# Optimization experiments

Measured on AMD Instinct MI355X. Metric: run time of the kernel, lower is better.

Reference implementation:

```python
import jax, jax.numpy as jnp
import numpy as np

D_MODEL = 512
N_HEADS = 8
HEAD_DIM = D_MODEL // N_HEADS
MAX_LEN = 250  # relative table has 2*MAX_LEN-1 = 499 rows
B, L = 2, 2048


def setup_inputs() -> dict:
    rng = jax.random.key(0)
    ks = jax.random.split(rng, 10)
    w = 1.0 / np.sqrt(D_MODEL)
    return {
        "query": jax.random.normal(ks[0], (B, L, D_MODEL), jnp.float32),
        "key": jax.random.normal(ks[1], (B, L, D_MODEL), jnp.float32),
        "value": jax.random.normal(ks[2], (B, L, D_MODEL), jnp.float32),
        "mask": jax.random.randint(ks[3], (B, L), 0, 2, jnp.int32),
        # weights stored as [in, out]; apply as x @ W + b (equivalent to torch Linear)
        "Wq": jax.random.normal(ks[4], (D_MODEL, D_MODEL), jnp.float32) * w,
        "bq": jnp.zeros((D_MODEL,), jnp.float32),
        "Wk": jax.random.normal(ks[5], (D_MODEL, D_MODEL), jnp.float32) * w,
        "bk": jnp.zeros((D_MODEL,), jnp.float32),
        "Wv": jax.random.normal(ks[6], (D_MODEL, D_MODEL), jnp.float32) * w,
        "bv": jnp.zeros((D_MODEL,), jnp.float32),
        "Wo": jax.random.normal(ks[7], (D_MODEL, D_MODEL), jnp.float32) * w,
        "bo": jnp.zeros((D_MODEL,), jnp.float32),
        "rel_table": jax.random.normal(ks[8], (2 * MAX_LEN - 1, HEAD_DIM), jnp.float32),
    }


def reference(query, key, value, mask, Wq, bq, Wk, bk, Wv, bv, Wo, bo, rel_table):
    b, l, d = query.shape
    hd = d // N_HEADS

    def split_heads(x):  # [b,l,d] -> [b,h,l,hd]
        return x.reshape(b, l, N_HEADS, hd).transpose(0, 2, 1, 3)

    Q = split_heads(query @ Wq + bq)
    K = split_heads(key @ Wk + bk)
    V = split_heads(value @ Wv + bv)

    scores = jnp.einsum('bhid,bhjd->bhij', Q, K) / jnp.sqrt(jnp.float32(hd))

    # relative position indices: idx[i,j] = clamp(j - i + MAX_LEN-1, 0, 2*MAX_LEN-2)
    pos = jnp.arange(l)
    idx = jnp.clip(pos[None, :] - pos[:, None] + MAX_LEN - 1, 0, 2 * MAX_LEN - 2)
    rel = rel_table[idx]  # [l, l, hd] gather
    # Shaw-style additive relative-position bias (per-pair scalar from Q . rel)
    scores = scores + jnp.einsum('bhid,ijd->bhij', Q, rel)

    # key-padding mask: [b,l] -> [b,1,1,l]
    scores = jnp.where(mask[:, None, None, :] == 0, jnp.float32(-1e10), scores)

    weights = jax.nn.softmax(scores, axis=-1)  # [b,h,l,l]
    out = jnp.einsum('bhij,bhjd->bhid', weights, V)
    out = out.transpose(0, 2, 1, 3).reshape(b, l, d)
    return out @ Wo + bo
```

## Files before the change

### kernel.cpp

```cpp
#include <hip/hip_runtime.h>
#include <math.h>

#define NREL 499
#define NREL_PAD 500
#define LDB 72
#define LDT 72

typedef __attribute__((ext_vector_type(8))) short bf16x8;
typedef __attribute__((ext_vector_type(4))) float f32x4;

__device__ __forceinline__ float bf2f(ushort x) {
  union { unsigned u; float f; } v; v.u = ((unsigned)x) << 16; return v.f;
}
__device__ __forceinline__ ushort f2bf(float x) {
  union { float f; unsigned u; } v; v.f = x;
  return (ushort)((v.u + 0x8000u) >> 16);
}
__device__ __forceinline__ bf16x8 pack8(float4 a, float4 b) {
  bf16x8 r;
  r[0] = (short)f2bf(a.x); r[1] = (short)f2bf(a.y);
  r[2] = (short)f2bf(a.z); r[3] = (short)f2bf(a.w);
  r[4] = (short)f2bf(b.x); r[5] = (short)f2bf(b.y);
  r[6] = (short)f2bf(b.z); r[7] = (short)f2bf(b.w);
  return r;
}

__global__ __launch_bounds__(256) void cast_bf16(const float* __restrict__ q,
                                                 const float* __restrict__ k,
                                                 const float* __restrict__ v,
                                                 ushort* __restrict__ dst) {
  const int z = blockIdx.z;
  const float* src = (z == 0) ? q : (z == 1) ? k : v;
  const size_t base = ((size_t)blockIdx.x * 256 + threadIdx.x) * 8;
  float4 a = *(const float4*)(src + base);
  float4 b = *(const float4*)(src + base + 4);
  *(bf16x8*)(dst + (size_t)z * 2097152 + base) = pack8(a, b);
}

__global__ __launch_bounds__(256) void prep_wt(const float* __restrict__ W0,
                                               const float* __restrict__ W1,
                                               const float* __restrict__ W2,
                                               const float* __restrict__ W3,
                                               const int* __restrict__ mask,
                                               ushort* __restrict__ Wt,
                                               ushort* __restrict__ maskbf) {
  __shared__ float T[64][68];
  const int t = threadIdx.x;
  const int k0 = blockIdx.x * 64, n0 = blockIdx.y * 64, z = blockIdx.z;
  const float* W = (z == 0) ? W0 : (z == 1) ? W1 : (z == 2) ? W2 : W3;
#pragma unroll
  for (int s = 0; s < 4; ++s) {
    int idx = t + s * 256;
    int r = idx >> 4, c4 = (idx & 15) << 2;
    *(float4*)&T[r][c4] = *(const float4*)(W + (size_t)(k0 + r) * 512 + n0 + c4);
  }
  if (blockIdx.x == 0 && blockIdx.y == 0) {
    int base = z * 1024 + t * 4;
    int4 mv = *(const int4*)(mask + base);
    ushort4 mo;
    mo.x = mv.x ? 0x3F80 : 0; mo.y = mv.y ? 0x3F80 : 0;
    mo.z = mv.z ? 0x3F80 : 0; mo.w = mv.w ? 0x3F80 : 0;
    *(ushort4*)(maskbf + base) = mo;
  }
  __syncthreads();
#pragma unroll
  for (int s = 0; s < 4; ++s) {
    int idx = t + s * 256;
    int row = idx >> 4, c4 = (idx & 15) << 2;
    ushort4 u = make_ushort4(f2bf(T[c4 + 0][row]), f2bf(T[c4 + 1][row]),
                             f2bf(T[c4 + 2][row]), f2bf(T[c4 + 3][row]));
    *(ushort4*)(Wt + (size_t)z * 262144 + (size_t)(n0 + row) * 512 + k0 + c4) = u;
  }
}

template <int MODE>
__device__ __forceinline__ void gemm_tile_body(const ushort* __restrict__ A,
                                               const ushort* __restrict__ Wt,
                                               const float* __restrict__ bias,
                                               const int* __restrict__ mvec,
                                               void* __restrict__ outv,
                                               int bx, int by, float oscale) {
  __shared__ ushort As[64 * LDT];
  __shared__ ushort Bs[64 * LDT];
  const int t = threadIdx.x;
  const int lane = t & 63, wave = t >> 6;
  const int m16 = lane & 15, quad = lane >> 4;
  const int koff = quad << 3;
  const int i0 = by * 64, n0 = bx * 64;
  const int row0 = t >> 3, off0 = (t & 7) << 3;
  const int row1 = (t + 256) >> 3, off1 = ((t + 256) & 7) << 3;
  const ushort* Ab = A + (size_t)i0 * 512;
  const ushort* Bb = Wt + (size_t)n0 * 512;

  uint4 ar0 = *(const uint4*)(Ab + (size_t)row0 * 512 + off0);
  uint4 ar1 = *(const uint4*)(Ab + (size_t)row1 * 512 + off1);
  uint4 br0 = *(const uint4*)(Bb + (size_t)row0 * 512 + off0);
  uint4 br1 = *(const uint4*)(Bb + (size_t)row1 * 512 + off1);

  f32x4 acc[4] = {{0.f, 0.f, 0.f, 0.f}, {0.f, 0.f, 0.f, 0.f},
                  {0.f, 0.f, 0.f, 0.f}, {0.f, 0.f, 0.f, 0.f}};

  for (int ks = 0; ks < 8; ++ks) {
    __syncthreads();
    *(uint4*)&As[row0 * LDT + off0] = ar0;
    *(uint4*)&As[row1 * LDT + off1] = ar1;
    *(uint4*)&Bs[row0 * LDT + off0] = br0;
    *(uint4*)&Bs[row1 * LDT + off1] = br1;
    __syncthreads();

    const int kn = ((ks + 1) & 7) << 6;
    uint4 an0 = *(const uint4*)(Ab + (size_t)row0 * 512 + kn + off0);
    uint4 an1 = *(const uint4*)(Ab + (size_t)row1 * 512 + kn + off1);
    uint4 bn0 = *(const uint4*)(Bb + (size_t)row0 * 512 + kn + off0);
    uint4 bn1 = *(const uint4*)(Bb + (size_t)row1 * 512 + kn + off1);

    __builtin_amdgcn_s_setprio(1);
    if (MODE != 1) {
#pragma unroll
      for (int kh = 0; kh < 2; ++kh) {
        bf16x8 af = *(const bf16x8*)&As[((wave << 4) + m16) * LDT + (kh << 5) + koff];
#pragma unroll
        for (int nt = 0; nt < 4; ++nt) {
          bf16x8 wf = *(const bf16x8*)&Bs[((nt << 4) + m16) * LDT + (kh << 5) + koff];
          acc[nt] = __builtin_amdgcn_mfma_f32_16x16x32_bf16(af, wf, acc[nt], 0, 0, 0);
        }
      }
    } else {
#pragma unroll
      for (int kh = 0; kh < 2; ++kh) {
        bf16x8 wf = *(const bf16x8*)&Bs[((wave << 4) + m16) * LDT + (kh << 5) + koff];
#pragma unroll
        for (int it = 0; it < 4; ++it) {
          bf16x8 af = *(const bf16x8*)&As[((it << 4) + m16) * LDT + (kh << 5) + koff];
          acc[it] = __builtin_amdgcn_mfma_f32_16x16x32_bf16(wf, af, acc[it], 0, 0, 0);
        }
      }
    }
    __builtin_amdgcn_s_setprio(0);

    ar0 = an0; ar1 = an1; br0 = bn0; br1 = bn1;
  }

  if (MODE == 0) {
    float* out = (float*)outv;
#pragma unroll
    for (int nt = 0; nt < 4; ++nt) {
      float bn = bias[n0 + (nt << 4) + m16];
#pragma unroll
      for (int r = 0; r < 4; ++r) {
        int i = i0 + (wave << 4) + (quad << 2) + r;
        out[(size_t)i * 512 + n0 + (nt << 4) + m16] = acc[nt][r] + bn;
      }
    }
  } else if (MODE == 2) {
    ushort* out = (ushort*)outv;
    const int b = i0 >> 11, l0 = i0 & 2047, h = n0 >> 6;
#pragma unroll
    for (int nt = 0; nt < 4; ++nt) {
      float bn = bias[n0 + (nt << 4) + m16];
      int d = (nt << 4) + m16;
#pragma unroll
      for (int r = 0; r < 4; ++r) {
        int il = (wave << 4) + (quad << 2) + r;
        out[((size_t)(b * 8 + h) * 2048 + l0 + il) * 64 + d] =
            f2bf((acc[nt][r] + bn) * oscale);
      }
    }
  } else {
    ushort* out = (ushort*)outv;
    const int b = i0 >> 11, l0 = i0 & 2047, h = n0 >> 6;
    float4 b4 = *(const float4*)(bias + n0 + (wave << 4) + (quad << 2));
    float bb[4] = {b4.x, b4.y, b4.z, b4.w};
    float mkf[4];
#pragma unroll
    for (int it = 0; it < 4; ++it)
      mkf[it] = (mvec[b * 2048 + l0 + (it << 4) + m16] != 0) ? 1.f : 0.f;
#pragma unroll
    for (int r = 0; r < 4; ++r) {
      int d = (wave << 4) + (quad << 2) + r;
#pragma unroll
      for (int it = 0; it < 4; ++it) {
        out[((size_t)(b * 8 + h) * 64 + d) * 2048 + l0 + (it << 4) + m16] =
            f2bf((acc[it][r] + bb[r]) * mkf[it]);
      }
    }
  }
}

template <int MODE>
__global__ __launch_bounds__(256) void gemm_tile(const ushort* __restrict__ A,
                                                 const ushort* __restrict__ Wt,
                                                 const float* __restrict__ bias,
                                                 void* __restrict__ outv) {
  gemm_tile_body<MODE>(A, Wt, bias, nullptr, outv, blockIdx.x, blockIdx.y, 1.f);
}

__global__ __launch_bounds__(256) void gemm_qkv(
    const ushort* __restrict__ Abf, const ushort* __restrict__ Wt,
    const float* __restrict__ bq, const float* __restrict__ bk,
    const float* __restrict__ bv, const int* __restrict__ mask,
    ushort* __restrict__ Qw, ushort* __restrict__ Kw, ushort* __restrict__ Vtw) {
  const int z = blockIdx.z;
  if (z == 0) {
    gemm_tile_body<2>(Abf, Wt, bq, nullptr, (void*)Qw, blockIdx.x, blockIdx.y,
                      0.125f);
  } else if (z == 1) {
    gemm_tile_body<2>(Abf + 2097152, Wt + 262144, bk, nullptr, (void*)Kw,
                      blockIdx.x, blockIdx.y, 1.f);
  } else {
    gemm_tile_body<1>(Abf + 2 * 2097152, Wt + 2 * 262144, bv, mask, (void*)Vtw,
                      blockIdx.x, blockIdx.y, 1.f);
  }
}

__global__ __launch_bounds__(256) void qrel_mfma(const ushort* __restrict__ Qw,
                                                 const float* __restrict__ rel,
                                                 float* __restrict__ qrel) {
  const int t = threadIdx.x;
  const int lane = t & 63, wave = t >> 6;
  const int m16 = lane & 15, quad = lane >> 4;
  const int r0 = blockIdx.x * 64;
  const int i0 = blockIdx.y * 64;
  const int bh = blockIdx.z;
  const ushort* Qb = Qw + ((size_t)bh * 2048 + i0 + (wave << 4) + m16) * 64;
  bf16x8 qa0 = *(const bf16x8*)(Qb + (quad << 3));
  bf16x8 qa1 = *(const bf16x8*)(Qb + 32 + (quad << 3));

  f32x4 acc[4] = {{0.f, 0.f, 0.f, 0.f}, {0.f, 0.f, 0.f, 0.f},
                  {0.f, 0.f, 0.f, 0.f}, {0.f, 0.f, 0.f, 0.f}};
#pragma unroll
  for (int rt = 0; rt < 4; ++rt) {
    int rr = min(r0 + (rt << 4) + m16, NREL - 1);
    const float* rp = rel + (size_t)rr * 64 + (quad << 3);
    float4 a0 = *(const float4*)rp,        a1 = *(const float4*)(rp + 4);
    float4 a2 = *(const float4*)(rp + 32), a3 = *(const float4*)(rp + 36);
    a0.x *= 8.f; a0.y *= 8.f; a0.z *= 8.f; a0.w *= 8.f;
    a1.x *= 8.f; a1.y *= 8.f; a1.z *= 8.f; a1.w *= 8.f;
    a2.x *= 8.f; a2.y *= 8.f; a2.z *= 8.f; a2.w *= 8.f;
    a3.x *= 8.f; a3.y *= 8.f; a3.z *= 8.f; a3.w *= 8.f;
    bf16x8 rf0 = pack8(a0, a1);
    bf16x8 rf1 = pack8(a2, a3);
    acc[rt] = __builtin_amdgcn_mfma_f32_16x16x32_bf16(qa0, rf0, acc[rt], 0, 0, 0);
    acc[rt] = __builtin_amdgcn_mfma_f32_16x16x32_bf16(qa1, rf1, acc[rt], 0, 0, 0);
  }
#pragma unroll
  for (int rt = 0; rt < 4; ++rt) {
    int r = r0 + (rt << 4) + m16;
    if (r < NREL_PAD) {
#pragma unroll
      for (int rg = 0; rg < 4; ++rg) {
        int i = i0 + (wave << 4) + (quad << 2) + rg;
        qrel[((size_t)bh * 2048 + i) * NREL_PAD + r] = acc[rt][rg];
      }
    }
  }
}

__device__ __forceinline__ void gather_qv(float qv[4][4],
                                          const float* __restrict__ qrow,
                                          int iq, int iw0, int j0, int quad) {
  if (j0 - iw0 >= 264) {
    float e = qrow[NREL - 1];
#pragma unroll
    for (int jt = 0; jt < 4; ++jt)
#pragma unroll
      for (int r = 0; r < 4; ++r) qv[jt][r] = e;
  } else if (iw0 - j0 >= 312) {
    float e = qrow[0];
#pragma unroll
    for (int jt = 0; jt < 4; ++jt)
#pragma unroll
      for (int r = 0; r < 4; ++r) qv[jt][r] = e;
  } else {
#pragma unroll
    for (int jt = 0; jt < 4; ++jt) {
#pragma unroll
      for (int r = 0; r < 4; ++r) {
        int j = j0 + (jt << 4) + (quad << 2) + r;
        int rr = min(NREL - 1, max(0, j - iq + 249));
        qv[jt][r] = qrow[rr];
      }
    }
  }
}

__global__ __launch_bounds__(256) void flash_attn(
    const ushort* __restrict__ Qw, const ushort* __restrict__ Kw,
    const ushort* __restrict__ Vt, const float* __restrict__ qrel,
    const ushort* __restrict__ maskbf, ushort* __restrict__ attnbf) {
  __shared__ ushort QPs[64 * LDB];
  __shared__ ushort Ks[64 * LDB];
  __shared__ ushort Vs[64 * LDB];
  const int t = threadIdx.x;
  const int lane = t & 63, wave = t >> 6;
  const int m16 = lane & 15, quad = lane >> 4;
  const int koff = quad << 3;
  const int bid = ((int)blockIdx.y << 5) + (int)blockIdx.x;
  const int swz = ((bid & 7) << 6) + (bid >> 3);
  const int i0 = (swz & 31) << 6;
  const int bh = swz >> 5;
  const int b = bh >> 3, h = bh & 7;
  const ushort* Qb = Qw + (size_t)bh * 2048 * 64;
  const ushort* Kb = Kw + (size_t)bh * 2048 * 64;
  const ushort* Vb = Vt + (size_t)bh * 64 * 2048;
  const ushort* mbf = maskbf + b * 2048;
  const int iw0 = i0 + (wave << 4);
  const int iq = iw0 + m16;
  const float* qrow = qrel + ((size_t)bh * 2048 + iq) * NREL_PAD;

  const int row0 = t >> 3, off0 = (t & 7) << 3;
  const int row1 = (t + 256) >> 3, off1 = ((t + 256) & 7) << 3;

  *(uint4*)&QPs[row0 * LDB + off0] =
      *(const uint4*)(Qb + (size_t)(i0 + row0) * 64 + off0);
  *(uint4*)&QPs[row1 * LDB + off1] =
      *(const uint4*)(Qb + (size_t)(i0 + row1) * 64 + off1);
  __syncthreads();

  bf16x8 qa0 = *(const bf16x8*)&QPs[((wave << 4) + m16) * LDB + koff];
  bf16x8 qa1 = *(const bf16x8*)&QPs[((wave << 4) + m16) * LDB + 32 + koff];

  uint4 kr0 = *(const uint4*)(Kb + (size_t)row0 * 64 + off0);
  uint4 kr1 = *(const uint4*)(Kb + (size_t)row1 * 64 + off1);
  uint4 vr0 = *(const uint4*)(Vb + (size_t)row0 * 2048 + off0);
  uint4 vr1 = *(const uint4*)(Vb + (size_t)row1 * 2048 + off1);
  bf16x8 mfr0 = *(const bf16x8*)(mbf + koff);
  bf16x8 mfr1 = *(const bf16x8*)(mbf + 32 + koff);
  float qv[4][4];
  gather_qv(qv, qrow, iq, iw0, 0, quad);

  float m_i = -INFINITY;
  f32x4 oacc[4];
  f32x4 lacc = {0.f, 0.f, 0.f, 0.f};
#pragma unroll
  for (int dt = 0; dt < 4; ++dt) oacc[dt] = (f32x4){0.f, 0.f, 0.f, 0.f};

  for (int j0 = 0; j0 < 2048; j0 += 64) {
    __syncthreads();
    *(uint4*)&Ks[row0 * LDB + off0] = kr0;
    *(uint4*)&Ks[row1 * LDB + off1] = kr1;
    *(uint4*)&Vs[row0 * LDB + off0] = vr0;
    *(uint4*)&Vs[row1 * LDB + off1] = vr1;
    __syncthreads();

    const int jn = (j0 + 64) & 2047;
    uint4 kn0 = *(const uint4*)(Kb + (size_t)(jn + row0) * 64 + off0);
    uint4 kn1 = *(const uint4*)(Kb + (size_t)(jn + row1) * 64 + off1);
    uint4 vn0 = *(const uint4*)(Vb + (size_t)row0 * 2048 + jn + off0);
    uint4 vn1 = *(const uint4*)(Vb + (size_t)row1 * 2048 + jn + off1);
    bf16x8 mfn0 = *(const bf16x8*)(mbf + jn + koff);
    bf16x8 mfn1 = *(const bf16x8*)(mbf + jn + 32 + koff);
    float qn[4][4];
    gather_qv(qn, qrow, iq, iw0, jn, quad);

    f32x4 sacc[4];
    __builtin_amdgcn_s_setprio(1);
#pragma unroll
    for (int jt = 0; jt < 4; ++jt) {
      bf16x8 kb0 = *(const bf16x8*)&Ks[((jt << 4) + m16) * LDB + koff];
      bf16x8 kb1 = *(const bf16x8*)&Ks[((jt << 4) + m16) * LDB + 32 + koff];
      f32x4 z = {qv[jt][0], qv[jt][1], qv[jt][2], qv[jt][3]};
      z = __builtin_amdgcn_mfma_f32_16x16x32_bf16(kb0, qa0, z, 0, 0, 0);
      z = __builtin_amdgcn_mfma_f32_16x16x32_bf16(kb1, qa1, z, 0, 0, 0);
      sacc[jt] = z;
    }
    __builtin_amdgcn_s_setprio(0);

    float t0 = fmaxf(fmaxf(sacc[0][0], sacc[0][1]), fmaxf(sacc[0][2], sacc[0][3]));
    float t1 = fmaxf(fmaxf(sacc[1][0], sacc[1][1]), fmaxf(sacc[1][2], sacc[1][3]));
    float t2 = fmaxf(fmaxf(sacc[2][0], sacc[2][1]), fmaxf(sacc[2][2], sacc[2][3]));
    float t3 = fmaxf(fmaxf(sacc[3][0], sacc[3][1]), fmaxf(sacc[3][2], sacc[3][3]));
    float mx = fmaxf(fmaxf(t0, t1), fmaxf(t2, t3));
    mx = fmaxf(mx, __shfl_xor(mx, 16));
    mx = fmaxf(mx, __shfl_xor(mx, 32));

    if (__any(mx > m_i + 8.f)) {
      float mnew = fmaxf(m_i, mx);
      float al = __expf(m_i - mnew);
      m_i = mnew;
#pragma unroll
      for (int dt = 0; dt < 4; ++dt)
#pragma unroll
        for (int r = 0; r < 4; ++r) oacc[dt][r] *= al;
#pragma unroll
      for (int r = 0; r < 4; ++r) lacc[r] *= al;
    }

    const int prow = ((wave << 4) + m16) * LDB;
#pragma unroll
    for (int jt = 0; jt < 4; ++jt) {
      ushort4 pk;
      pk.x = f2bf(__expf(sacc[jt][0] - m_i));
      pk.y = f2bf(__expf(sacc[jt][1] - m_i));
      pk.z = f2bf(__expf(sacc[jt][2] - m_i));
      pk.w = f2bf(__expf(sacc[jt][3] - m_i));
      *(ushort4*)&QPs[prow + (jt << 4) + (quad << 2)] = pk;
    }
    __asm__ volatile("s_waitcnt lgkmcnt(0)" ::: "memory");

    bf16x8 pa0 = *(const bf16x8*)&QPs[prow + koff];
    bf16x8 pa1 = *(const bf16x8*)&QPs[prow + 32 + koff];
    __builtin_amdgcn_s_setprio(1);
    lacc = __builtin_amdgcn_mfma_f32_16x16x32_bf16(mfr0, pa0, lacc, 0, 0, 0);
    lacc = __builtin_amdgcn_mfma_f32_16x16x32_bf16(mfr1, pa1, lacc, 0, 0, 0);
#pragma unroll
    for (int dt = 0; dt < 4; ++dt) {
      bf16x8 vb0 = *(const bf16x8*)&Vs[((dt << 4) + m16) * LDB + koff];
      bf16x8 vb1 = *(const bf16x8*)&Vs[((dt << 4) + m16) * LDB + 32 + koff];
      oacc[dt] = __builtin_amdgcn_mfma_f32_16x16x32_bf16(vb0, pa0, oacc[dt], 0, 0, 0);
      oacc[dt] = __builtin_amdgcn_mfma_f32_16x16x32_bf16(vb1, pa1, oacc[dt], 0, 0, 0);
    }
    __builtin_amdgcn_s_setprio(0);

    kr0 = kn0; kr1 = kn1; vr0 = vn0; vr1 = vn1;
    mfr0 = mfn0; mfr1 = mfn1;
#pragma unroll
    for (int jt = 0; jt < 4; ++jt)
#pragma unroll
      for (int r = 0; r < 4; ++r) qv[jt][r] = qn[jt][r];
  }

  float inv = 1.0f / lacc[0];
  ushort* dst = attnbf + (size_t)(b * 2048 + iq) * 512 + h * 64;
#pragma unroll
  for (int dt = 0; dt < 4; ++dt) {
    ushort4 st;
    st.x = f2bf(oacc[dt][0] * inv);
    st.y = f2bf(oacc[dt][1] * inv);
    st.z = f2bf(oacc[dt][2] * inv);
    st.w = f2bf(oacc[dt][3] * inv);
    *(ushort4*)(dst + (dt << 4) + (quad << 2)) = st;
  }
}

extern "C" void kernel_launch(void* const* d_in, const int* in_sizes, int n_in,
                              void* d_out, int out_size, void* d_ws,
                              size_t ws_size, hipStream_t stream) {
  const float* query = (const float*)d_in[0];
  const float* key   = (const float*)d_in[1];
  const float* value = (const float*)d_in[2];
  const int*   mask  = (const int*)d_in[3];
  const float* Wq = (const float*)d_in[4];
  const float* bq = (const float*)d_in[5];
  const float* Wk = (const float*)d_in[6];
  const float* bk = (const float*)d_in[7];
  const float* Wv = (const float*)d_in[8];
  const float* bv = (const float*)d_in[9];
  const float* Wo = (const float*)d_in[10];
  const float* bo = (const float*)d_in[11];
  const float* rel = (const float*)d_in[12];

  char* w = (char*)d_ws;
  size_t off = 0;
  ushort* Qw  = (ushort*)(w + off); off += (size_t)16 * 2048 * 64 * 2;
  ushort* Kw  = (ushort*)(w + off); off += (size_t)16 * 2048 * 64 * 2;
  ushort* Vtw = (ushort*)(w + off); off += (size_t)16 * 64 * 2048 * 2;
  ushort* Wt  = (ushort*)(w + off); off += (size_t)4 * 512 * 512 * 2;
  float* qrel = (float*)(w + off);  off += (size_t)16 * 2048 * NREL_PAD * 4;
  ushort* attnbf = (ushort*)(w + off); off += (size_t)4096 * 512 * 2;
  ushort* Abf = (ushort*)(w + off); off += (size_t)3 * 4096 * 512 * 2;
  ushort* maskbf = (ushort*)(w + off); off += (size_t)2 * 2048 * 2;
  float* out = (float*)d_out;

  dim3 bb(256);
  hipLaunchKernelGGL(cast_bf16, dim3(1024, 1, 3), bb, 0, stream, query, key,
                     value, Abf);
  hipLaunchKernelGGL(prep_wt, dim3(8, 8, 4), bb, 0, stream, Wq, Wk, Wv, Wo,
                     mask, Wt, maskbf);
  hipLaunchKernelGGL(gemm_qkv, dim3(8, 64, 3), bb, 0, stream, Abf, Wt, bq, bk,
                     bv, mask, Qw, Kw, Vtw);
  hipLaunchKernelGGL(qrel_mfma, dim3(8, 32, 16), bb, 0, stream, Qw, rel, qrel);
  hipLaunchKernelGGL(flash_attn, dim3(32, 16), bb, 0, stream, Qw, Kw, Vtw, qrel,
                     maskbf, attnbf);
  hipLaunchKernelGGL((gemm_tile<0>), dim3(8, 64), bb, 0, stream, attnbf,
                     Wt + 3 * 262144, bo, (void*)out);
}
```

Measured before the change: 232.1 us.

## Fuse fp32-to-bf16 input cast into QKV GEMM and load K/V fragments directly

Removes the separate cast kernel: the QKV projection GEMM now reads fp32 inputs and converts them to bf16 while staging into shared memory, which saves a kernel launch and a full round trip of the activations. Flash attention no longer stages Q, K and V through shared memory. Each wave loads its MFMA fragments straight from global memory (K is prefetched one tile ahead, V is loaded per tile), which removes the block-wide barriers and frees LDS. Launch bounds ask for 2 blocks per SM. The trade-off is more redundant global and L2 traffic, since each wave now reloads the same K/V rows, and higher register pressure from the fragment arrays.

After: 296.6 us. 1.28x slower.

```diff
diff --git a/kernel.cpp b/kernel.cpp
--- a/kernel.cpp
+++ b/kernel.cpp
@@ -23,18 +23,6 @@
   r[4] = (short)f2bf(b.x); r[5] = (short)f2bf(b.y);
   r[6] = (short)f2bf(b.z); r[7] = (short)f2bf(b.w);
   return r;
-}
-
-__global__ __launch_bounds__(256) void cast_bf16(const float* __restrict__ q,
-                                                 const float* __restrict__ k,
-                                                 const float* __restrict__ v,
-                                                 ushort* __restrict__ dst) {
-  const int z = blockIdx.z;
-  const float* src = (z == 0) ? q : (z == 1) ? k : v;
-  const size_t base = ((size_t)blockIdx.x * 256 + threadIdx.x) * 8;
-  float4 a = *(const float4*)(src + base);
-  float4 b = *(const float4*)(src + base + 4);
-  *(bf16x8*)(dst + (size_t)z * 2097152 + base) = pack8(a, b);
 }
 
 __global__ __launch_bounds__(256) void prep_wt(const float* __restrict__ W0,
@@ -73,8 +61,8 @@
   }
 }
 
-template <int MODE>
-__device__ __forceinline__ void gemm_tile_body(const ushort* __restrict__ A,
+template <int MODE, int AFP32>
+__device__ __forceinline__ void gemm_tile_body(const void* __restrict__ Av,
                                                const ushort* __restrict__ Wt,
                                                const float* __restrict__ bias,
                                                const int* __restrict__ mvec,
@@ -89,11 +77,21 @@
   const int i0 = by * 64, n0 = bx * 64;
   const int row0 = t >> 3, off0 = (t & 7) << 3;
   const int row1 = (t + 256) >> 3, off1 = ((t + 256) & 7) << 3;
-  const ushort* Ab = A + (size_t)i0 * 512;
+  const ushort* Ab16 = (const ushort*)Av + (size_t)i0 * 512;
+  const float*  Ab32 = (const float*)Av + (size_t)i0 * 512;
   const ushort* Bb = Wt + (size_t)n0 * 512;
 
-  uint4 ar0 = *(const uint4*)(Ab + (size_t)row0 * 512 + off0);
-  uint4 ar1 = *(const uint4*)(Ab + (size_t)row1 * 512 + off1);
+  uint4 ar0, ar1;
+  float4 af00, af01, af10, af11;
+  if (AFP32) {
+    af00 = *(const float4*)(Ab32 + (size_t)row0 * 512 + off0);
+    af01 = *(const float4*)(Ab32 + (size_t)row0 * 512 + off0 + 4);
+    af10 = *(const float4*)(Ab32 + (size_t)row1 * 512 + off1);
+    af11 = *(const float4*)(Ab32 + (size_t)row1 * 512 + off1 + 4);
+  } else {
+    ar0 = *(const uint4*)(Ab16 + (size_t)row0 * 512 + off0);
+    ar1 = *(const uint4*)(Ab16 + (size_t)row1 * 512 + off1);
+  }
   uint4 br0 = *(const uint4*)(Bb + (size_t)row0 * 512 + off0);
   uint4 br1 = *(const uint4*)(Bb + (size_t)row1 * 512 + off1);
 
@@ -102,17 +100,29 @@
 
   for (int ks = 0; ks < 8; ++ks) {
     __syncthreads();
-    *(uint4*)&As[row0 * LDT + off0] = ar0;
-    *(uint4*)&As[row1 * LDT + off1] = ar1;
+    if (AFP32) {
+      *(bf16x8*)&As[row0 * LDT + off0] = pack8(af00, af01);
+      *(bf16x8*)&As[row1 * LDT + off1] = pack8(af10, af11);
+    } else {
+      *(uint4*)&As[row0 * LDT + off0] = ar0;
+      *(uint4*)&As[row1 * LDT + off1] = ar1;
+    }
     *(uint4*)&Bs[row0 * LDT + off0] = br0;
     *(uint4*)&Bs[row1 * LDT + off1] = br1;
     __syncthreads();
 
     const int kn = ((ks + 1) & 7) << 6;
-    uint4 an0 = *(const uint4*)(Ab + (size_t)row0 * 512 + kn + off0);
-    uint4 an1 = *(const uint4*)(Ab + (size_t)row1 * 512 + kn + off1);
-    uint4 bn0 = *(const uint4*)(Bb + (size_t)row0 * 512 + kn + off0);
-    uint4 bn1 = *(const uint4*)(Bb + (size_t)row1 * 512 + kn + off1);
+    if (AFP32) {
+      af00 = *(const float4*)(Ab32 + (size_t)row0 * 512 + kn + off0);
+      af01 = *(const float4*)(Ab32 + (size_t)row0 * 512 + kn + off0 + 4);
+      af10 = *(const float4*)(Ab32 + (size_t)row1 * 512 + kn + off1);
+      af11 = *(const float4*)(Ab32 + (size_t)row1 * 512 + kn + off1 + 4);
+    } else {
+      ar0 = *(const uint4*)(Ab16 + (size_t)row0 * 512 + kn + off0);
+      ar1 = *(const uint4*)(Ab16 + (size_t)row1 * 512 + kn + off1);
+    }
+    br0 = *(const uint4*)(Bb + (size_t)row0 * 512 + kn + off0);
+    br1 = *(const uint4*)(Bb + (size_t)row1 * 512 + kn + off1);
 
     __builtin_amdgcn_s_setprio(1);
     if (MODE != 1) {
@@ -137,8 +147,6 @@
       }
     }
     __builtin_amdgcn_s_setprio(0);
-
-    ar0 = an0; ar1 = an1; br0 = bn0; br1 = bn1;
   }
 
   if (MODE == 0) {
@@ -187,29 +195,31 @@
   }
 }
 
-template <int MODE>
-__global__ __launch_bounds__(256) void gemm_tile(const ushort* __restrict__ A,
+template <int MODE, int AFP32>
+__global__ __launch_bounds__(256) void gemm_tile(const void* __restrict__ A,
                                                  const ushort* __restrict__ Wt,
                                                  const float* __restrict__ bias,
                                                  void* __restrict__ outv) {
-  gemm_tile_body<MODE>(A, Wt, bias, nullptr, outv, blockIdx.x, blockIdx.y, 1.f);
+  gemm_tile_body<MODE, AFP32>(A, Wt, bias, nullptr, outv, blockIdx.x,
+                              blockIdx.y, 1.f);
 }
 
 __global__ __launch_bounds__(256) void gemm_qkv(
-    const ushort* __restrict__ Abf, const ushort* __restrict__ Wt,
+    const float* __restrict__ q, const float* __restrict__ k,
+    const float* __restrict__ v, const ushort* __restrict__ Wt,
     const float* __restrict__ bq, const float* __restrict__ bk,
     const float* __restrict__ bv, const int* __restrict__ mask,
     ushort* __restrict__ Qw, ushort* __restrict__ Kw, ushort* __restrict__ Vtw) {
   const int z = blockIdx.z;
   if (z == 0) {
-    gemm_tile_body<2>(Abf, Wt, bq, nullptr, (void*)Qw, blockIdx.x, blockIdx.y,
-                      0.125f);
+    gemm_tile_body<2, 1>(q, Wt, bq, nullptr, (void*)Qw, blockIdx.x, blockIdx.y,
+                         0.125f);
   } else if (z == 1) {
-    gemm_tile_body<2>(Abf + 2097152, Wt + 262144, bk, nullptr, (void*)Kw,
-                      blockIdx.x, blockIdx.y, 1.f);
+    gemm_tile_body<2, 1>(k, Wt + 262144, bk, nullptr, (void*)Kw, blockIdx.x,
+                         blockIdx.y, 1.f);
   } else {
-    gemm_tile_body<1>(Abf + 2 * 2097152, Wt + 2 * 262144, bv, mask, (void*)Vtw,
-                      blockIdx.x, blockIdx.y, 1.f);
+    gemm_tile_body<1, 1>(v, Wt + 2 * 262144, bv, mask, (void*)Vtw, blockIdx.x,
+                         blockIdx.y, 1.f);
   }
 }
 
@@ -258,19 +268,18 @@
 
 __device__ __forceinline__ void gather_qv(float qv[4][4],
                                           const float* __restrict__ qrow,
+                                          float e_lo, float e_hi,
                                           int iq, int iw0, int j0, int quad) {
   if (j0 - iw0 >= 264) {
-    float e = qrow[NREL - 1];
 #pragma unroll
     for (int jt = 0; jt < 4; ++jt)
 #pragma unroll
-      for (int r = 0; r < 4; ++r) qv[jt][r] = e;
+      for (int r = 0; r < 4; ++r) qv[jt][r] = e_hi;
   } else if (iw0 - j0 >= 312) {
-    float e = qrow[0];
 #pragma unroll
     for (int jt = 0; jt < 4; ++jt)
 #pragma unroll
-      for (int r = 0; r < 4; ++r) qv[jt][r] = e;
+      for (int r = 0; r < 4; ++r) qv[jt][r] = e_lo;
   } else {
 #pragma unroll
     for (int jt = 0; jt < 4; ++jt) {
@@ -284,13 +293,11 @@
   }
 }
 
-__global__ __launch_bounds__(256) void flash_attn(
+__global__ __launch_bounds__(256, 2) void flash_attn(
     const ushort* __restrict__ Qw, const ushort* __restrict__ Kw,
     const ushort* __restrict__ Vt, const float* __restrict__ qrel,
     const ushort* __restrict__ maskbf, ushort* __restrict__ attnbf) {
-  __shared__ ushort QPs[64 * LDB];
-  __shared__ ushort Ks[64 * LDB];
-  __shared__ ushort Vs[64 * LDB];
+  __shared__ ushort Ps[64 * LDB];
   const int t = threadIdx.x;
   const int lane = t & 63, wave = t >> 6;
   const int m16 = lane & 15, quad = lane >> 4;
@@ -300,71 +307,69 @@
   const int i0 = (swz & 31) << 6;
   const int bh = swz >> 5;
   const int b = bh >> 3, h = bh & 7;
-  const ushort* Qb = Qw + (size_t)bh * 2048 * 64;
   const ushort* Kb = Kw + (size_t)bh * 2048 * 64;
   const ushort* Vb = Vt + (size_t)bh * 64 * 2048;
   const ushort* mbf = maskbf + b * 2048;
   const int iw0 = i0 + (wave << 4);
   const int iq = iw0 + m16;
   const float* qrow = qrel + ((size_t)bh * 2048 + iq) * NREL_PAD;
-
-  const int row0 = t >> 3, off0 = (t & 7) << 3;
-  const int row1 = (t + 256) >> 3, off1 = ((t + 256) & 7) << 3;
-
-  *(uint4*)&QPs[row0 * LDB + off0] =
-      *(const uint4*)(Qb + (size_t)(i0 + row0) * 64 + off0);
-  *(uint4*)&QPs[row1 * LDB + off1] =
-      *(const uint4*)(Qb + (size_t)(i0 + row1) * 64 + off1);
-  __syncthreads();
-
-  bf16x8 qa0 = *(const bf16x8*)&QPs[((wave << 4) + m16) * LDB + koff];
-  bf16x8 qa1 = *(const bf16x8*)&QPs[((wave << 4) + m16) * LDB + 32 + koff];
-
-  uint4 kr0 = *(const uint4*)(Kb + (size_t)row0 * 64 + off0);
-  uint4 kr1 = *(const uint4*)(Kb + (size_t)row1 * 64 + off1);
-  uint4 vr0 = *(const uint4*)(Vb + (size_t)row0 * 2048 + off0);
-  uint4 vr1 = *(const uint4*)(Vb + (size_t)row1 * 2048 + off1);
-  bf16x8 mfr0 = *(const bf16x8*)(mbf + koff);
-  bf16x8 mfr1 = *(const bf16x8*)(mbf + 32 + koff);
-  float qv[4][4];
-  gather_qv(qv, qrow, iq, iw0, 0, quad);
+  const float e_lo = qrow[0], e_hi = qrow[NREL - 1];
+
+  const ushort* qp = Qw + ((size_t)bh * 2048 + iq) * 64 + koff;
+  bf16x8 qa0 = *(const bf16x8*)qp;
+  bf16x8 qa1 = *(const bf16x8*)(qp + 32);
+
+  bf16x8 kf[8];
+#pragma unroll
+  for (int jt = 0; jt < 4; ++jt) {
+    const ushort* kp = Kb + (size_t)((jt << 4) + m16) * 64 + koff;
+    kf[jt * 2]     = *(const bf16x8*)kp;
+    kf[jt * 2 + 1] = *(const bf16x8*)(kp + 32);
+  }
 
   float m_i = -INFINITY;
   f32x4 oacc[4];
   f32x4 lacc = {0.f, 0.f, 0.f, 0.f};
 #pragma unroll
   for (int dt = 0; dt < 4; ++dt) oacc[dt] = (f32x4){0.f, 0.f, 0.f, 0.f};
+  const int prow = ((wave << 4) + m16) * LDB;
 
   for (int j0 = 0; j0 < 2048; j0 += 64) {
-    __syncthreads();
-    *(uint4*)&Ks[row0 * LDB + off0] = kr0;
-    *(uint4*)&Ks[row1 * LDB + off1] = kr1;
-    *(uint4*)&Vs[row0 * LDB + off0] = vr0;
-    *(uint4*)&Vs[row1 * LDB + off1] = vr1;
-    __syncthreads();
-
-    const int jn = (j0 + 64) & 2047;
-    uint4 kn0 = *(const uint4*)(Kb + (size_t)(jn + row0) * 64 + off0);
-    uint4 kn1 = *(const uint4*)(Kb + (size_t)(jn + row1) * 64 + off1);
-    uint4 vn0 = *(const uint4*)(Vb + (size_t)row0 * 2048 + jn + off0);
-    uint4 vn1 = *(const uint4*)(Vb + (size_t)row1 * 2048 + jn + off1);
-    bf16x8 mfn0 = *(const bf16x8*)(mbf + jn + koff);
-    bf16x8 mfn1 = *(const bf16x8*)(mbf + jn + 32 + koff);
-    float qn[4][4];
-    gather_qv(qn, qrow, iq, iw0, jn, quad);
+    bf16x8 vf[8];
+#pragma unroll
+    for (int dt = 0; dt < 4; ++dt) {
+      const ushort* vp = Vb + (size_t)((dt << 4) + m16) * 2048 + j0 + koff;
+      vf[dt * 2]     = *(const bf16x8*)vp;
+      vf[dt * 2 + 1] = *(const bf16x8*)(vp + 32);
+    }
+    bf16x8 mf0 = *(const bf16x8*)(mbf + j0 + koff);
+    bf16x8 mf1 = *(const bf16x8*)(mbf + j0 + 32 + koff);
+    float qv[4][4];
+    gather_qv(qv, qrow, e_lo, e_hi, iq, iw0, j0, quad);
 
     f32x4 sacc[4];
     __builtin_amdgcn_s_setprio(1);
 #pragma unroll
     for (int jt = 0; jt < 4; ++jt) {
-      bf16x8 kb0 = *(const bf16x8*)&Ks[((jt << 4) + m16) * LDB + koff];
-      bf16x8 kb1 = *(const bf16x8*)&Ks[((jt << 4) + m16) * LDB + 32 + koff];
-      f32x4 z = {qv[jt][0], qv[jt][1], qv[jt][2], qv[jt][3]};
-      z = __builtin_amdgcn_mfma_f32_16x16x32_bf16(kb0, qa0, z, 0, 0, 0);
-      z = __builtin_amdgcn_mfma_f32_16x16x32_bf16(kb1, qa1, z, 0, 0, 0);
+      f32x4 z = {0.f, 0.f, 0.f, 0.f};
+      z = __builtin_amdgcn_mfma_f32_16x16x32_bf16(kf[jt * 2], qa0, z, 0, 0, 0);
+      z = __builtin_amdgcn_mfma_f32_16x16x32_bf16(kf[jt * 2 + 1], qa1, z, 0, 0, 0);
       sacc[jt] = z;
     }
     __builtin_amdgcn_s_setprio(0);
+
+    const int jn = (j0 + 64) & 2047;
+#pragma unroll
+    for (int jt = 0; jt < 4; ++jt) {
+      const ushort* kp = Kb + (size_t)(jn + (jt << 4) + m16) * 64 + koff;
+      kf[jt * 2]     = *(const bf16x8*)kp;
+      kf[jt * 2 + 1] = *(const bf16x8*)(kp + 32);
+    }
+
+#pragma unroll
+    for (int jt = 0; jt < 4; ++jt)
+#pragma unroll
+      for (int r = 0; r < 4; ++r) sacc[jt][r] += qv[jt][r];
 
     float t0 = fmaxf(fmaxf(sacc[0][0], sacc[0][1]), fmaxf(sacc[0][2], sacc[0][3]));
     float t1 = fmaxf(fmaxf(sacc[1][0], sacc[1][1]), fmaxf(sacc[1][2], sacc[1][3]));
@@ -386,7 +391,6 @@
       for (int r = 0; r < 4; ++r) lacc[r] *= al;
     }
 
-    const int prow = ((wave << 4) + m16) * LDB;
 #pragma unroll
     for (int jt = 0; jt < 4; ++jt) {
       ushort4 pk;
@@ -394,30 +398,21 @@
       pk.y = f2bf(__expf(sacc[jt][1] - m_i));
       pk.z = f2bf(__expf(sacc[jt][2] - m_i));
       pk.w = f2bf(__expf(sacc[jt][3] - m_i));
-      *(ushort4*)&QPs[prow + (jt << 4) + (quad << 2)] = pk;
+      *(ushort4*)&Ps[prow + (jt << 4) + (quad << 2)] = pk;
     }
     __asm__ volatile("s_waitcnt lgkmcnt(0)" ::: "memory");
 
-    bf16x8 pa0 = *(const bf16x8*)&QPs[prow + koff];
-    bf16x8 pa1 = *(const bf16x8*)&QPs[prow + 32 + koff];
+    bf16x8 pa0 = *(const bf16x8*)&Ps[prow + koff];
+    bf16x8 pa1 = *(const bf16x8*)&Ps[prow + 32 + koff];
     __builtin_amdgcn_s_setprio(1);
-    lacc = __builtin_amdgcn_mfma_f32_16x16x32_bf16(mfr0, pa0, lacc, 0, 0, 0);
-    lacc = __builtin_amdgcn_mfma_f32_16x16x32_bf16(mfr1, pa1, lacc, 0, 0, 0);
+    lacc = __builtin_amdgcn_mfma_f32_16x16x32_bf16(mf0, pa0, lacc, 0, 0, 0);
+    lacc = __builtin_amdgcn_mfma_f32_16x16x32_bf16(mf1, pa1, lacc, 0, 0, 0);
 #pragma unroll
     for (int dt = 0; dt < 4; ++dt) {
-      bf16x8 vb0 = *(const bf16x8*)&Vs[((dt << 4) + m16) * LDB + koff];
-      bf16x8 vb1 = *(const bf16x8*)&Vs[((dt << 4) + m16) * LDB + 32 + koff];
-      oacc[dt] = __builtin_amdgcn_mfma_f32_16x16x32_bf16(vb0, pa0, oacc[dt], 0, 0, 0);
-      oacc[dt] = __builtin_amdgcn_mfma_f32_16x16x32_bf16(vb1, pa1, oacc[dt], 0, 0, 0);
+      oacc[dt] = __builtin_amdgcn_mfma_f32_16x16x32_bf16(vf[dt * 2], pa0, oacc[dt], 0, 0, 0);
+      oacc[dt] = __builtin_amdgcn_mfma_f32_16x16x32_bf16(vf[dt * 2 + 1], pa1, oacc[dt], 0, 0, 0);
     }
     __builtin_amdgcn_s_setprio(0);
-
-    kr0 = kn0; kr1 = kn1; vr0 = vn0; vr1 = vn1;
-    mfr0 = mfn0; mfr1 = mfn1;
-#pragma unroll
-    for (int jt = 0; jt < 4; ++jt)
-#pragma unroll
-      for (int r = 0; r < 4; ++r) qv[jt][r] = qn[jt][r];
   }
 
   float inv = 1.0f / lacc[0];
@@ -458,20 +453,17 @@
   ushort* Wt  = (ushort*)(w + off); off += (size_t)4 * 512 * 512 * 2;
   float* qrel = (float*)(w + off);  off += (size_t)16 * 2048 * NREL_PAD * 4;
   ushort* attnbf = (ushort*)(w + off); off += (size_t)4096 * 512 * 2;
-  ushort* Abf = (ushort*)(w + off); off += (size_t)3 * 4096 * 512 * 2;
   ushort* maskbf = (ushort*)(w + off); off += (size_t)2 * 2048 * 2;
   float* out = (float*)d_out;
 
   dim3 bb(256);
-  hipLaunchKernelGGL(cast_bf16, dim3(1024, 1, 3), bb, 0, stream, query, key,
-                     value, Abf);
   hipLaunchKernelGGL(prep_wt, dim3(8, 8, 4), bb, 0, stream, Wq, Wk, Wv, Wo,
                      mask, Wt, maskbf);
-  hipLaunchKernelGGL(gemm_qkv, dim3(8, 64, 3), bb, 0, stream, Abf, Wt, bq, bk,
-                     bv, mask, Qw, Kw, Vtw);
+  hipLaunchKernelGGL(gemm_qkv, dim3(8, 64, 3), bb, 0, stream, query, key, value,
+                     Wt, bq, bk, bv, mask, Qw, Kw, Vtw);
   hipLaunchKernelGGL(qrel_mfma, dim3(8, 32, 16), bb, 0, stream, Qw, rel, qrel);
   hipLaunchKernelGGL(flash_attn, dim3(32, 16), bb, 0, stream, Qw, Kw, Vtw, qrel,
                      maskbf, attnbf);
-  hipLaunchKernelGGL((gemm_tile<0>), dim3(8, 64), bb, 0, stream, attnbf,
+  hipLaunchKernelGGL((gemm_tile<0, 0>), dim3(8, 64), bb, 0, stream, attnbf,
                      Wt + 3 * 262144, bo, (void*)out);
 }
```
